# Performance work log

Measured on AMD Instinct MI355X. Metric: run time of the kernel, lower is better.

Reference implementation:

```python
import jax, jax.numpy as jnp
import numpy as np


def setup_inputs() -> dict:
    key = jax.random.key(0)
    k_x, k_enc, k_dec = jax.random.split(key, 3)
    B, T, d_in, d_sae = 2048, 4, 768, 16384
    x = jax.random.normal(k_x, (B, T, d_in), dtype=jnp.float32)
    W_enc = jax.random.normal(k_enc, (T, d_in, d_sae), dtype=jnp.float32) * (1.0 / d_in ** 0.5)
    W_dec = jax.random.normal(k_dec, (d_sae, T, d_in), dtype=jnp.float32) * (1.0 / d_sae ** 0.5)
    b_enc = jnp.zeros((d_sae,), dtype=jnp.float32)
    b_dec = jnp.zeros((T, d_in), dtype=jnp.float32)
    return {"x": x, "W_enc": W_enc, "b_enc": b_enc, "W_dec": W_dec, "b_dec": b_dec, "k": 128}


def reference(x, W_enc, b_enc, W_dec, b_dec, k):
    # pre-activations: (B, d_sae)
    pre = jnp.einsum('btd,tds->bs', x, W_enc) + b_enc
    # top-k selection along dictionary dim, then relu + scatter into zero vector
    vals, idx = jax.lax.top_k(pre, k)                      # (B, k)
    B = pre.shape[0]
    rows = jnp.arange(B)[:, None]                          # (B, 1)
    z = jnp.zeros_like(pre).at[rows, idx].set(jax.nn.relu(vals))  # (B, d_sae)
    # dense decode (original ignores sparsity of z)
    x_hat = jnp.einsum('bs,std->btd', z, W_dec) + b_dec    # (B, T, d_in)
    recon_loss = jnp.mean(jnp.sum((x_hat - x) ** 2, axis=-1))
    return (recon_loss, x_hat, z)
```

## Files before the change

kernel.cpp:

```cpp
#include <hip/hip_runtime.h>
#include <hip/hip_bf16.h>

#define B_ROWS 2048
#define K_DIM  3072
#define N_DIM  16384
#define TOPK   128
#define XHAT_ELEMS (B_ROWS * K_DIM)

typedef __bf16 bf16x8 __attribute__((ext_vector_type(8)));
typedef float  f32x4  __attribute__((ext_vector_type(4)));

#define LDSTRIDE 40

__device__ __forceinline__ unsigned bf16rne(float f) {
    unsigned u = __float_as_uint(f);
    unsigned r = u + 0x7fffu + ((u >> 16) & 1u);
    return r & 0xffff0000u;
}
__device__ __forceinline__ unsigned pk2_rne(float x, float y) {
    return (bf16rne(x) >> 16) | bf16rne(y);
}
__device__ __forceinline__ float lo16f(unsigned u) { return __uint_as_float(u << 16); }
__device__ __forceinline__ float hi16f(unsigned u) { return __uint_as_float(u & 0xffff0000u); }

__device__ __forceinline__ int swz4(int r) { return (r ^ (r >> 2)) & 3; }

__device__ __forceinline__ void gl_lds16(const void* g, void* l) {
    __builtin_amdgcn_global_load_lds((__attribute__((address_space(1))) const void*)g,
                                     (__attribute__((address_space(3))) void*)l, 16, 0, 0);
}

__global__ __launch_bounds__(256) void split_x_kernel(const float* __restrict__ X,
                                                      unsigned short* __restrict__ Xh,
                                                      unsigned short* __restrict__ Xl) {
    size_t i = ((size_t)blockIdx.x * 256 + threadIdx.x) * 8;
    float4 a = *(const float4*)(X + i);
    float4 b = *(const float4*)(X + i + 4);
    unsigned h0 = pk2_rne(a.x, a.y), h1 = pk2_rne(a.z, a.w);
    unsigned h2 = pk2_rne(b.x, b.y), h3 = pk2_rne(b.z, b.w);
    unsigned l0 = pk2_rne(a.x - lo16f(h0), a.y - hi16f(h0));
    unsigned l1 = pk2_rne(a.z - lo16f(h1), a.w - hi16f(h1));
    unsigned l2 = pk2_rne(b.x - lo16f(h2), b.y - hi16f(h2));
    unsigned l3 = pk2_rne(b.z - lo16f(h3), b.w - hi16f(h3));
    uint4 hv; hv.x = h0; hv.y = h1; hv.z = h2; hv.w = h3;
    uint4 lv; lv.x = l0; lv.y = l1; lv.z = l2; lv.w = l3;
    *(uint4*)(Xh + i) = hv;
    *(uint4*)(Xl + i) = lv;
}

__global__ __launch_bounds__(256) void split_wT_kernel(const float* __restrict__ W,
                                                       unsigned short* __restrict__ WhT,
                                                       unsigned short* __restrict__ WlT) {
    __shared__ float s[64][65];
    const int t  = threadIdx.x;
    const int k0 = blockIdx.x * 64;
    const int n0 = blockIdx.y * 64;
    const int c4 = t & 15, r = t >> 4;

#pragma unroll
    for (int p = 0; p < 4; ++p) {
        int rr = r + p * 16;
        float4 v = *(const float4*)(W + (size_t)(k0 + rr) * N_DIM + n0 + c4 * 4);
        s[rr][c4 * 4 + 0] = v.x;
        s[rr][c4 * 4 + 1] = v.y;
        s[rr][c4 * 4 + 2] = v.z;
        s[rr][c4 * 4 + 3] = v.w;
    }
    __syncthreads();
#pragma unroll
    for (int p = 0; p < 4; ++p) {
        int rr = r + p * 16;
        float v0 = s[c4 * 4 + 0][rr];
        float v1 = s[c4 * 4 + 1][rr];
        float v2 = s[c4 * 4 + 2][rr];
        float v3 = s[c4 * 4 + 3][rr];
        unsigned h01 = pk2_rne(v0, v1), h23 = pk2_rne(v2, v3);
        unsigned l01 = pk2_rne(v0 - lo16f(h01), v1 - hi16f(h01));
        unsigned l23 = pk2_rne(v2 - lo16f(h23), v3 - hi16f(h23));
        size_t o = (size_t)(n0 + rr) * K_DIM + k0 + c4 * 4;
        uint2 hv; hv.x = h01; hv.y = h23;
        uint2 lv; lv.x = l01; lv.y = l23;
        *(uint2*)(WhT + o) = hv;
        *(uint2*)(WlT + o) = lv;
    }
}

__global__ __launch_bounds__(256) void enc_gemm_presplit(
        const unsigned short* __restrict__ Xh, const unsigned short* __restrict__ Xl,
        const unsigned short* __restrict__ WhT, const unsigned short* __restrict__ WlT,
        const float* __restrict__ benc, float* __restrict__ pre) {
    __shared__ unsigned short Ah[128 * 32], Al[128 * 32];
    __shared__ unsigned short Bh[128 * 32], Bl[128 * 32];

    const int t   = threadIdx.x;
    const int bid = blockIdx.x;
    const int mt  = bid & 15;
    const int nt  = bid >> 4;
    const int m0  = mt * 128, n0 = nt * 128;

    const int sr = t >> 2;
    const int sc = ((t & 3) ^ swz4(sr)) * 8;
    const size_t rstep = (size_t)64 * K_DIM;

    const unsigned short* xh0 = Xh  + (size_t)(m0 + sr) * K_DIM + sc;
    const unsigned short* xl0 = Xl  + (size_t)(m0 + sr) * K_DIM + sc;
    const unsigned short* wh0 = WhT + (size_t)(n0 + sr) * K_DIM + sc;
    const unsigned short* wl0 = WlT + (size_t)(n0 + sr) * K_DIM + sc;

    unsigned short* ahD0 = &Ah[(size_t)t * 8];
    unsigned short* ahD1 = &Ah[(size_t)(t + 256) * 8];
    unsigned short* alD0 = &Al[(size_t)t * 8];
    unsigned short* alD1 = &Al[(size_t)(t + 256) * 8];
    unsigned short* bhD0 = &Bh[(size_t)t * 8];
    unsigned short* bhD1 = &Bh[(size_t)(t + 256) * 8];
    unsigned short* blD0 = &Bl[(size_t)t * 8];
    unsigned short* blD1 = &Bl[(size_t)(t + 256) * 8];

    f32x4 acc[4][4];
#pragma unroll
    for (int mi = 0; mi < 4; ++mi)
#pragma unroll
        for (int ni = 0; ni < 4; ++ni) acc[mi][ni] = (f32x4)0.f;

    const int w = t >> 6, lane = t & 63;
    const int wm = (w >> 1) * 64, wn = (w & 1) * 64;
    const int fm = lane & 15, fk = lane >> 4;
    const int koff = (fk ^ swz4(fm)) * 8;

    for (int k0 = 0; k0 < K_DIM; k0 += 32) {
        __syncthreads();
        gl_lds16(xh0 + k0,         ahD0);
        gl_lds16(xh0 + k0 + rstep, ahD1);
        gl_lds16(xl0 + k0,         alD0);
        gl_lds16(xl0 + k0 + rstep, alD1);
        gl_lds16(wh0 + k0,         bhD0);
        gl_lds16(wh0 + k0 + rstep, bhD1);
        gl_lds16(wl0 + k0,         blD0);
        gl_lds16(wl0 + k0 + rstep, blD1);
        __syncthreads();

        bf16x8 aH[4], aL[4];
#pragma unroll
        for (int mi = 0; mi < 4; ++mi) {
            int r = (wm + mi * 16 + fm) * 32 + koff;
            aH[mi] = *(const bf16x8*)&Ah[r];
            aL[mi] = *(const bf16x8*)&Al[r];
        }
#pragma unroll
        for (int ni = 0; ni < 4; ++ni) {
            int r = (wn + ni * 16 + fm) * 32 + koff;
            bf16x8 bH = *(const bf16x8*)&Bh[r];
            bf16x8 bL = *(const bf16x8*)&Bl[r];
#pragma unroll
            for (int mi = 0; mi < 4; ++mi) {
                acc[mi][ni] = __builtin_amdgcn_mfma_f32_16x16x32_bf16(aH[mi], bH, acc[mi][ni], 0, 0, 0);
                acc[mi][ni] = __builtin_amdgcn_mfma_f32_16x16x32_bf16(aH[mi], bL, acc[mi][ni], 0, 0, 0);
                acc[mi][ni] = __builtin_amdgcn_mfma_f32_16x16x32_bf16(aL[mi], bH, acc[mi][ni], 0, 0, 0);
            }
        }
    }

    const int frow = fk * 4, fcol = fm;
#pragma unroll
    for (int ni = 0; ni < 4; ++ni) {
        int col = n0 + wn + ni * 16 + fcol;
        float bv = benc[col];
#pragma unroll
        for (int mi = 0; mi < 4; ++mi) {
            int row = m0 + wm + mi * 16 + frow;
            float* p = pre + (size_t)row * N_DIM + col;
#pragma unroll
            for (int r = 0; r < 4; ++r) p[(size_t)r * N_DIM] = acc[mi][ni][r] + bv;
        }
    }
}

__global__ __launch_bounds__(256) void enc_gemm_mfma(const float* __restrict__ X,
                                                     const float* __restrict__ W,
                                                     const float* __restrict__ benc,
                                                     float* __restrict__ pre) {
    __shared__ unsigned short Ahi[128 * LDSTRIDE], Alo[128 * LDSTRIDE];
    __shared__ unsigned short Bhi[128 * LDSTRIDE], Blo[128 * LDSTRIDE];

    const int t   = threadIdx.x;
    const int bid = blockIdx.x;
    const int mt  = bid & 15;
    const int nt  = bid >> 4;
    const int m0  = mt * 128, n0 = nt * 128;

    int am[4], akq[4], bn[4], bkq[4];
    const float* Xp[4];
    const float* Wp[4];
#pragma unroll
    for (int i = 0; i < 4; ++i) {
        int id = t + 256 * i;
        am[i]  = id >> 3;
        akq[i] = id & 7;
        Xp[i]  = X + (size_t)(m0 + am[i]) * K_DIM + akq[i] * 4;
        bn[i]  = id & 127;
        bkq[i] = id >> 7;
        Wp[i]  = W + (size_t)(bkq[i] * 4) * N_DIM + n0 + bn[i];
    }

    f32x4 acc[4][4];
#pragma unroll
    for (int mi = 0; mi < 4; ++mi)
#pragma unroll
        for (int ni = 0; ni < 4; ++ni) acc[mi][ni] = (f32x4)0.f;

    float4 aR[4];
    float  bR[4][4];
#pragma unroll
    for (int i = 0; i < 4; ++i) {
        aR[i] = *(const float4*)(Xp[i]);
#pragma unroll
        for (int j = 0; j < 4; ++j) bR[i][j] = Wp[i][(size_t)j * N_DIM];
    }

    const int w = t >> 6, lane = t & 63;
    const int wm = (w >> 1) * 64, wn = (w & 1) * 64;
    const int fm = lane & 15, fk = lane >> 4;

    for (int k0 = 0; k0 < K_DIM; k0 += 32) {
        __syncthreads();
#pragma unroll
        for (int i = 0; i < 4; ++i) {
            float4 v = aR[i];
            unsigned h0 = pk2_rne(v.x, v.y), h1 = pk2_rne(v.z, v.w);
            unsigned l0 = pk2_rne(v.x - lo16f(h0), v.y - hi16f(h0));
            unsigned l1 = pk2_rne(v.z - lo16f(h1), v.w - hi16f(h1));
            int off = am[i] * LDSTRIDE + akq[i] * 4;
            uint2 uh; uh.x = h0; uh.y = h1;
            uint2 ul; ul.x = l0; ul.y = l1;
            *(uint2*)&Ahi[off] = uh;
            *(uint2*)&Alo[off] = ul;

            float w0 = bR[i][0], w1 = bR[i][1], w2 = bR[i][2], w3 = bR[i][3];
            unsigned g0 = pk2_rne(w0, w1), g1 = pk2_rne(w2, w3);
            unsigned m0u = pk2_rne(w0 - lo16f(g0), w1 - hi16f(g0));
            unsigned m1u = pk2_rne(w2 - lo16f(g1), w3 - hi16f(g1));
            int boff = bn[i] * LDSTRIDE + bkq[i] * 4;
            uint2 gh; gh.x = g0; gh.y = g1;
            uint2 gl; gl.x = m0u; gl.y = m1u;
            *(uint2*)&Bhi[boff] = gh;
            *(uint2*)&Blo[boff] = gl;
        }
        __syncthreads();

        if (k0 + 32 < K_DIM) {
#pragma unroll
            for (int i = 0; i < 4; ++i) {
                aR[i] = *(const float4*)(Xp[i] + (k0 + 32));
                const float* p = Wp[i] + (size_t)(k0 + 32) * N_DIM;
#pragma unroll
                for (int j = 0; j < 4; ++j) bR[i][j] = p[(size_t)j * N_DIM];
            }
        }

        bf16x8 aH[4], aL[4];
#pragma unroll
        for (int mi = 0; mi < 4; ++mi) {
            int r = (wm + mi * 16 + fm) * LDSTRIDE + fk * 8;
            aH[mi] = *(const bf16x8*)&Ahi[r];
            aL[mi] = *(const bf16x8*)&Alo[r];
        }
#pragma unroll
        for (int ni = 0; ni < 4; ++ni) {
            int r = (wn + ni * 16 + fm) * LDSTRIDE + fk * 8;
            bf16x8 bH = *(const bf16x8*)&Bhi[r];
            bf16x8 bL = *(const bf16x8*)&Blo[r];
#pragma unroll
            for (int mi = 0; mi < 4; ++mi) {
                acc[mi][ni] = __builtin_amdgcn_mfma_f32_16x16x32_bf16(aH[mi], bH, acc[mi][ni], 0, 0, 0);
                acc[mi][ni] = __builtin_amdgcn_mfma_f32_16x16x32_bf16(aH[mi], bL, acc[mi][ni], 0, 0, 0);
                acc[mi][ni] = __builtin_amdgcn_mfma_f32_16x16x32_bf16(aL[mi], bH, acc[mi][ni], 0, 0, 0);
            }
        }
    }

    const int frow = fk * 4, fcol = fm;
#pragma unroll
    for (int ni = 0; ni < 4; ++ni) {
        int col = n0 + wn + ni * 16 + fcol;
        float bv = benc[col];
#pragma unroll
        for (int mi = 0; mi < 4; ++mi) {
            int row = m0 + wm + mi * 16 + frow;
            float* p = pre + (size_t)row * N_DIM + col;
#pragma unroll
            for (int r = 0; r < 4; ++r) p[(size_t)r * N_DIM] = acc[mi][ni][r] + bv;
        }
    }
}

__device__ __forceinline__ unsigned sortkey(float f) {
    unsigned u = __float_as_uint(f);
    return (u & 0x80000000u) ? ~u : (u | 0x80000000u);
}

__device__ __forceinline__ int wave_red_int(int v) {
#pragma unroll
    for (int o = 32; o > 0; o >>= 1) v += __shfl_xor(v, o);
    return v;
}

__global__ __launch_bounds__(256) void topk_kernel(float* __restrict__ z,
                                                   int* __restrict__ oIdx,
                                                   float* __restrict__ oVal) {
    __shared__ unsigned short k16[N_DIM];
    __shared__ int s4[4];
    __shared__ int s_candN;
    __shared__ int s_candIdx[256];
    __shared__ unsigned s_candKey[256];
    __shared__ int s_quota;
    __shared__ int s_outPos;

    const int row = blockIdx.x;
    const int t = threadIdx.x;
    float* zr = z + (size_t)row * N_DIM;

    if (t == 0) { s_candN = 0; s_outPos = 0; }

    for (int i = t; i < N_DIM; i += 256) {
        k16[i] = (unsigned short)(sortkey(zr[i]) >> 16);
    }
    __syncthreads();

    unsigned cur = 0;
    for (int bit = 15; bit >= 0; --bit) {
        unsigned cand = cur | (1u << bit);
        int c = 0;
        for (int i = t; i < N_DIM; i += 256) c += (k16[i] >= cand) ? 1 : 0;
        c = wave_red_int(c);
        __syncthreads();
        if ((t & 63) == 0) s4[t >> 6] = c;
        __syncthreads();
        int total = s4[0] + s4[1] + s4[2] + s4[3];
        if (total >= TOPK) cur = cand;
    }

    {
        int c = 0;
        for (int i = t; i < N_DIM; i += 256) c += (k16[i] > cur) ? 1 : 0;
        c = wave_red_int(c);
        __syncthreads();
        if ((t & 63) == 0) s4[t >> 6] = c;
        __syncthreads();
        int cgt = s4[0] + s4[1] + s4[2] + s4[3];
        if (t == 0) s_quota = TOPK - cgt;
    }
    __syncthreads();

    for (int i = t; i < N_DIM; i += 256) {
        if (k16[i] == (unsigned short)cur) {
            int p = atomicAdd(&s_candN, 1);
            if (p < 256) {
                s_candIdx[p] = i;
                s_candKey[p] = sortkey(zr[i]);
            }
        }
    }
    __syncthreads();

    if (t == 0) {
        int n = s_candN < 256 ? s_candN : 256;
        int q = s_quota;
        if (q > n) q = n;
        s_quota = q;
        for (int a = 0; a < q; ++a) {
            int best = a;
            for (int b = a + 1; b < n; ++b) {
                if (s_candKey[b] > s_candKey[best] ||
                    (s_candKey[b] == s_candKey[best] && s_candIdx[b] < s_candIdx[best]))
                    best = b;
            }
            if (best != a) {
                unsigned tk = s_candKey[a]; s_candKey[a] = s_candKey[best]; s_candKey[best] = tk;
                int ti = s_candIdx[a]; s_candIdx[a] = s_candIdx[best]; s_candIdx[best] = ti;
            }
        }
    }
    __syncthreads();

    const int quota = s_quota;
    for (int i = t; i < N_DIM; i += 256) {
        float f = zr[i];
        unsigned short kk = k16[i];
        bool sel = kk > (unsigned short)cur;
        if (!sel && kk == (unsigned short)cur) {
            for (int j = 0; j < quota; ++j)
                if (s_candIdx[j] == i) { sel = true; break; }
        }
        float zv = sel ? fmaxf(f, 0.f) : 0.f;
        zr[i] = zv;
        if (sel) {
            int p = atomicAdd(&s_outPos, 1);
            oIdx[row * TOPK + p] = i;
            oVal[row * TOPK + p] = zv;
        }
    }
}

__global__ __launch_bounds__(256) void decode_kernel(const int* __restrict__ idxL,
                                                     const float* __restrict__ valL,
                                                     const float* __restrict__ Wdec,
                                                     const float* __restrict__ bdec,
                                                     const float* __restrict__ x,
                                                     float* __restrict__ xhat,
                                                     float* __restrict__ loss) {
    __shared__ int s_idx[TOPK];
    __shared__ float s_val[TOPK];
    __shared__ float sred[4];

    const int row = blockIdx.x;
    const int t = threadIdx.x;

    if (t < TOPK) {
        s_idx[t] = idxL[row * TOPK + t];
        s_val[t] = valL[row * TOPK + t];
    }
    __syncthreads();

    float acc[12];
#pragma unroll
    for (int e = 0; e < 12; ++e) acc[e] = bdec[t + e * 256];

    for (int i = 0; i < TOPK; ++i) {
        const float v = s_val[i];
        const float* wr = Wdec + (size_t)s_idx[i] * K_DIM;
#pragma unroll
        for (int e = 0; e < 12; ++e)
            acc[e] = fmaf(v, wr[t + e * 256], acc[e]);
    }

    const float* xr = x + (size_t)row * K_DIM;
    float* xo = xhat + (size_t)row * K_DIM;
    float part = 0.f;
#pragma unroll
    for (int e = 0; e < 12; ++e) {
        float d = acc[e] - xr[t + e * 256];
        part = fmaf(d, d, part);
        xo[t + e * 256] = acc[e];
    }

#pragma unroll
    for (int o = 32; o > 0; o >>= 1) part += __shfl_xor(part, o);
    if ((t & 63) == 0) sred[t >> 6] = part;
    __syncthreads();
    if (t == 0) {
        float total = sred[0] + sred[1] + sred[2] + sred[3];
        atomicAdd(loss, total * (1.0f / 8192.0f));
    }
}

extern "C" void kernel_launch(void* const* d_in, const int* in_sizes, int n_in,
                              void* d_out, int out_size, void* d_ws, size_t ws_size,
                              hipStream_t stream) {
    const float* x     = (const float*)d_in[0];
    const float* W_enc = (const float*)d_in[1];
    const float* b_enc = (const float*)d_in[2];
    const float* W_dec = (const float*)d_in[3];
    const float* b_dec = (const float*)d_in[4];

    float* out  = (float*)d_out;
    float* loss = out;
    float* xhat = out + 1;
    float* z    = out + 1 + XHAT_ELEMS;

    const size_t idxB   = (size_t)B_ROWS * TOPK * sizeof(int);
    const size_t planeW = (size_t)K_DIM * N_DIM * 2;
    const size_t planeX = (size_t)B_ROWS * K_DIM * 2;
    const size_t need   = 2 * idxB + 2 * planeW + 2 * planeX;

    int*   oIdx = (int*)d_ws;
    float* oVal = (float*)((char*)d_ws + idxB);

    (void)hipMemsetAsync(loss, 0, sizeof(float), stream);

    if (ws_size >= need) {
        unsigned short* WhT = (unsigned short*)((char*)d_ws + 2 * idxB);
        unsigned short* WlT = (unsigned short*)((char*)WhT + planeW);
        unsigned short* Xh  = (unsigned short*)((char*)WlT + planeW);
        unsigned short* Xl  = (unsigned short*)((char*)Xh + planeX);

        split_x_kernel<<<(B_ROWS * K_DIM) / (8 * 256), 256, 0, stream>>>(x, Xh, Xl);
        split_wT_kernel<<<dim3(K_DIM / 64, N_DIM / 64), 256, 0, stream>>>(W_enc, WhT, WlT);
        enc_gemm_presplit<<<2048, 256, 0, stream>>>(Xh, Xl, WhT, WlT, b_enc, z);
    } else {
        enc_gemm_mfma<<<2048, 256, 0, stream>>>(x, W_enc, b_enc, z);
    }

    topk_kernel<<<B_ROWS, 256, 0, stream>>>(z, oIdx, oVal);

    decode_kernel<<<B_ROWS, 256, 0, stream>>>(oIdx, oVal, W_dec, b_dec, x, xhat, loss);
}
```

Before: 1.607 ms.

## Rewrite presplit encoder GEMM with 256x256 tiles, double-buffered LDS and phased prefetch

The split-bf16 encoder GEMM now uses 512-thread blocks computing 256x256 output tiles, with hi/lo planes interleaved in one XOR-swizzled LDS buffer. The next K-slice is double-buffered and its loads are issued in four phases between MFMA groups, using explicit vmcnt waits and raw barriers plus s_setprio around the MFMA bursts. Blocks are also remapped for locality. The aim is to hide global-to-LDS latency and raise operand reuse per load, at the cost of more registers (8x4 accumulators) and about 128KB of LDS, which leaves one block per CU.

```diff
diff --git a/kernel.cpp b/kernel.cpp
--- a/kernel.cpp
+++ b/kernel.cpp
@@ -22,8 +22,6 @@
 }
 __device__ __forceinline__ float lo16f(unsigned u) { return __uint_as_float(u << 16); }
 __device__ __forceinline__ float hi16f(unsigned u) { return __uint_as_float(u & 0xffff0000u); }
-
-__device__ __forceinline__ int swz4(int r) { return (r ^ (r >> 2)) & 3; }
 
 __device__ __forceinline__ void gl_lds16(const void* g, void* l) {
     __builtin_amdgcn_global_load_lds((__attribute__((address_space(1))) const void*)g,
@@ -85,89 +83,131 @@
     }
 }
 
-__global__ __launch_bounds__(256) void enc_gemm_presplit(
+#define BK 32
+#define NT (K_DIM / BK)
+
+__global__ __launch_bounds__(512) void enc_gemm_8ph(
         const unsigned short* __restrict__ Xh, const unsigned short* __restrict__ Xl,
         const unsigned short* __restrict__ WhT, const unsigned short* __restrict__ WlT,
         const float* __restrict__ benc, float* __restrict__ pre) {
-    __shared__ unsigned short Ah[128 * 32], Al[128 * 32];
-    __shared__ unsigned short Bh[128 * 32], Bl[128 * 32];
-
-    const int t   = threadIdx.x;
-    const int bid = blockIdx.x;
-    const int mt  = bid & 15;
-    const int nt  = bid >> 4;
-    const int m0  = mt * 128, n0 = nt * 128;
-
-    const int sr = t >> 2;
-    const int sc = ((t & 3) ^ swz4(sr)) * 8;
-    const size_t rstep = (size_t)64 * K_DIM;
-
-    const unsigned short* xh0 = Xh  + (size_t)(m0 + sr) * K_DIM + sc;
-    const unsigned short* xl0 = Xl  + (size_t)(m0 + sr) * K_DIM + sc;
-    const unsigned short* wh0 = WhT + (size_t)(n0 + sr) * K_DIM + sc;
-    const unsigned short* wl0 = WlT + (size_t)(n0 + sr) * K_DIM + sc;
-
-    unsigned short* ahD0 = &Ah[(size_t)t * 8];
-    unsigned short* ahD1 = &Ah[(size_t)(t + 256) * 8];
-    unsigned short* alD0 = &Al[(size_t)t * 8];
-    unsigned short* alD1 = &Al[(size_t)(t + 256) * 8];
-    unsigned short* bhD0 = &Bh[(size_t)t * 8];
-    unsigned short* bhD1 = &Bh[(size_t)(t + 256) * 8];
-    unsigned short* blD0 = &Bl[(size_t)t * 8];
-    unsigned short* blD1 = &Bl[(size_t)(t + 256) * 8];
-
-    f32x4 acc[4][4];
-#pragma unroll
-    for (int mi = 0; mi < 4; ++mi)
+    __shared__ unsigned short Ap[2][256 * 64];
+    __shared__ unsigned short Bp[2][256 * 64];
+
+    const int t = threadIdx.x;
+    const int b = blockIdx.x;
+    const int wg = (b & 7) * 64 + (b >> 3);
+    const int mt = wg & 7, nt = wg >> 3;
+    const int m0 = mt * 256, n0 = nt * 256;
+
+    const unsigned short* srcP[8];
+    unsigned short* dstP[8];
+#pragma unroll
+    for (int j = 0; j < 8; ++j) {
+        int g = j * 512 + t;
+        int r = (g >> 3) & 255;
+        int s = g & 7;
+        int c = s ^ (r & 7);
+        if (j < 4) {
+            const unsigned short* base = (c & 4) ? Xl : Xh;
+            srcP[j] = base + (size_t)(m0 + r) * K_DIM + (c & 3) * 8;
+            dstP[j] = &Ap[0][(g & 2047) * 8];
+        } else {
+            const unsigned short* base = (c & 4) ? WlT : WhT;
+            srcP[j] = base + (size_t)(n0 + r) * K_DIM + (c & 3) * 8;
+            dstP[j] = &Bp[0][(g & 2047) * 8];
+        }
+    }
+
+    f32x4 acc[8][4];
+#pragma unroll
+    for (int mi = 0; mi < 8; ++mi)
 #pragma unroll
         for (int ni = 0; ni < 4; ++ni) acc[mi][ni] = (f32x4)0.f;
 
     const int w = t >> 6, lane = t & 63;
-    const int wm = (w >> 1) * 64, wn = (w & 1) * 64;
+    const int wr = w >> 2, wc = w & 3;
     const int fm = lane & 15, fk = lane >> 4;
-    const int koff = (fk ^ swz4(fm)) * 8;
-
-    for (int k0 = 0; k0 < K_DIM; k0 += 32) {
-        __syncthreads();
-        gl_lds16(xh0 + k0,         ahD0);
-        gl_lds16(xh0 + k0 + rstep, ahD1);
-        gl_lds16(xl0 + k0,         alD0);
-        gl_lds16(xl0 + k0 + rstep, alD1);
-        gl_lds16(wh0 + k0,         bhD0);
-        gl_lds16(wh0 + k0 + rstep, bhD1);
-        gl_lds16(wl0 + k0,         blD0);
-        gl_lds16(wl0 + k0 + rstep, blD1);
-        __syncthreads();
-
-        bf16x8 aH[4], aL[4];
-#pragma unroll
-        for (int mi = 0; mi < 4; ++mi) {
-            int r = (wm + mi * 16 + fm) * 32 + koff;
-            aH[mi] = *(const bf16x8*)&Ah[r];
-            aL[mi] = *(const bf16x8*)&Al[r];
+
+#pragma unroll
+    for (int j = 0; j < 8; ++j) gl_lds16(srcP[j], dstP[j]);
+
+#define APHASE(P)                                                                   \
+    {                                                                               \
+        _Pragma("unroll")                                                           \
+        for (int q = 0; q < 2; ++q) {                                               \
+            int r = wr * 128 + (2 * (P) + q) * 16 + fm;                             \
+            int off = r * 64 + (fk ^ (r & 7)) * 8;                                  \
+            aHf[q] = *(const bf16x8*)&Ap[cur][off];                                 \
+            aLf[q] = *(const bf16x8*)&Ap[cur][off ^ 32];                            \
+        }                                                                           \
+        __builtin_amdgcn_s_setprio(1);                                              \
+        _Pragma("unroll")                                                           \
+        for (int q = 0; q < 2; ++q) {                                               \
+            _Pragma("unroll")                                                       \
+            for (int ni = 0; ni < 4; ++ni) {                                        \
+                acc[2*(P)+q][ni] = __builtin_amdgcn_mfma_f32_16x16x32_bf16(aHf[q], bHf[ni], acc[2*(P)+q][ni], 0, 0, 0); \
+                acc[2*(P)+q][ni] = __builtin_amdgcn_mfma_f32_16x16x32_bf16(aHf[q], bLf[ni], acc[2*(P)+q][ni], 0, 0, 0); \
+                acc[2*(P)+q][ni] = __builtin_amdgcn_mfma_f32_16x16x32_bf16(aLf[q], bHf[ni], acc[2*(P)+q][ni], 0, 0, 0); \
+            }                                                                       \
+        }                                                                           \
+        __builtin_amdgcn_s_setprio(0);                                              \
+        asm volatile("s_barrier" ::: "memory");                                     \
+    }
+
+    int cur = 0;
+    for (int kt = 0; kt < NT; ++kt) {
+        const int kOff = (kt + 1) * BK;
+        const int nb = cur ^ 1;
+        const int nbO = nb * (256 * 64);
+        const bool notLast = (kt + 1 < NT);
+
+        bf16x8 bHf[4], bLf[4], aHf[2], aLf[2];
+
+        if (notLast) {
+            gl_lds16(srcP[0] + kOff, dstP[0] + nbO);
+            gl_lds16(srcP[1] + kOff, dstP[1] + nbO);
+            asm volatile("s_waitcnt vmcnt(2)\n\ts_barrier" ::: "memory");
+        } else {
+            asm volatile("s_waitcnt vmcnt(0)\n\ts_barrier" ::: "memory");
         }
 #pragma unroll
         for (int ni = 0; ni < 4; ++ni) {
-            int r = (wn + ni * 16 + fm) * 32 + koff;
-            bf16x8 bH = *(const bf16x8*)&Bh[r];
-            bf16x8 bL = *(const bf16x8*)&Bl[r];
-#pragma unroll
-            for (int mi = 0; mi < 4; ++mi) {
-                acc[mi][ni] = __builtin_amdgcn_mfma_f32_16x16x32_bf16(aH[mi], bH, acc[mi][ni], 0, 0, 0);
-                acc[mi][ni] = __builtin_amdgcn_mfma_f32_16x16x32_bf16(aH[mi], bL, acc[mi][ni], 0, 0, 0);
-                acc[mi][ni] = __builtin_amdgcn_mfma_f32_16x16x32_bf16(aL[mi], bH, acc[mi][ni], 0, 0, 0);
-            }
-        }
-    }
-
-    const int frow = fk * 4, fcol = fm;
+            int r = wc * 64 + ni * 16 + fm;
+            int off = r * 64 + (fk ^ (r & 7)) * 8;
+            bHf[ni] = *(const bf16x8*)&Bp[cur][off];
+            bLf[ni] = *(const bf16x8*)&Bp[cur][off ^ 32];
+        }
+        APHASE(0)
+
+        if (notLast) {
+            gl_lds16(srcP[2] + kOff, dstP[2] + nbO);
+            gl_lds16(srcP[3] + kOff, dstP[3] + nbO);
+        }
+        APHASE(1)
+
+        if (notLast) {
+            gl_lds16(srcP[4] + kOff, dstP[4] + nbO);
+            gl_lds16(srcP[5] + kOff, dstP[5] + nbO);
+        }
+        APHASE(2)
+
+        if (notLast) {
+            gl_lds16(srcP[6] + kOff, dstP[6] + nbO);
+            gl_lds16(srcP[7] + kOff, dstP[7] + nbO);
+        }
+        APHASE(3)
+
+        cur = nb;
+    }
+#undef APHASE
+
 #pragma unroll
     for (int ni = 0; ni < 4; ++ni) {
-        int col = n0 + wn + ni * 16 + fcol;
+        int col = n0 + wc * 64 + ni * 16 + fm;
         float bv = benc[col];
 #pragma unroll
-        for (int mi = 0; mi < 4; ++mi) {
-            int row = m0 + wm + mi * 16 + frow;
+        for (int mi = 0; mi < 8; ++mi) {
+            int row = m0 + wr * 128 + mi * 16 + fk * 4;
             float* p = pre + (size_t)row * N_DIM + col;
 #pragma unroll
             for (int r = 0; r < 4; ++r) p[(size_t)r * N_DIM] = acc[mi][ni][r] + bv;
@@ -485,7 +525,7 @@
 
         split_x_kernel<<<(B_ROWS * K_DIM) / (8 * 256), 256, 0, stream>>>(x, Xh, Xl);
         split_wT_kernel<<<dim3(K_DIM / 64, N_DIM / 64), 256, 0, stream>>>(W_enc, WhT, WlT);
-        enc_gemm_presplit<<<2048, 256, 0, stream>>>(Xh, Xl, WhT, WlT, b_enc, z);
+        enc_gemm_8ph<<<512, 512, 0, stream>>>(Xh, Xl, WhT, WlT, b_enc, z);
     } else {
         enc_gemm_mfma<<<2048, 256, 0, stream>>>(x, W_enc, b_enc, z);
     }
```

Result: faster. 1.567 ms (-2.5%).
